# Optimization experiments

Hardware: AMD Instinct MI355X
Metric: run time of the kernel (lower is better)

The kernel has to match this reference:

```python
import jax, jax.numpy as jnp
import numpy as np

EPS = 1e-4
GRID_RES = 0.01
L = 2
ATOL = 0.01
RTOL = 1e-5


def compute_lub(f_v, edges):
    # f_v: [V,2] vertex filtration values; edges: [E,2] int vertex indices
    e_x = jnp.max(f_v[:, 0][edges], axis=1)  # [E]
    e_y = jnp.max(f_v[:, 1][edges], axis=1)  # [E]
    f_e = jnp.stack([e_x, e_y], axis=1) + EPS  # [E,2]
    return jnp.concatenate([f_v, f_e], axis=0)  # [V+E, 2] = [S,2]


def grad_matrices(filtration, bar, sample_pts):
    # filtration: [S,2], bar: [P,R], sample_pts: [P,2]
    # Vectorized version of the per-point Python loops in moveSimplices.forward.
    S = filtration.shape[0]
    P = sample_pts.shape[0]
    fx, fy = filtration[:, 0], filtration[:, 1]          # [S]
    px, py = sample_pts[:, 0], sample_pts[:, 1]          # [P]
    fsum = fx + fy                                        # [S]
    psum = px + py                                        # [P]
    shift = jnp.arange(-L, L + 1, dtype=filtration.dtype)  # [5]
    tol_x = ATOL + RTOL * jnp.abs(fx)                     # torch.isclose tolerance
    tol_y = ATOL + RTOL * jnp.abs(fy)
    below = fsum[None, :] < psum[:, None]                 # [P,S]
    above = fsum[None, :] > psum[:, None]

    Gs, Gcs = [], []
    for r in range(bar.shape[1]):  # small fixed rank loop (R=3)
        s = bar[:, r] + GRID_RES                          # [P]
        line_x = shift[None, :] * s[:, None] + px[:, None]  # [P,5]
        line_y = shift[None, :] * s[:, None] + py[:, None]
        last_x, last_y = line_x[:, -1], line_y[:, -1]      # [P] (shift=+L endpoint)
        # isclose over shifts, reduced with any() (duplicate scatter writes are idempotent)
        hit_x = (jnp.abs(line_x[:, None, :] - fx[None, :, None]) <= tol_x[None, :, None]).any(-1)  # [P,S]
        hit_y = (jnp.abs(line_y[:, None, :] - fy[None, :, None]) <= tol_y[None, :, None]).any(-1)
        lx = hit_x & (fy[None, :] <= last_y[:, None]) & below
        ux = hit_x & (fy[None, :] <= last_y[:, None]) & above
        ly = hit_y & (fx[None, :] <= last_x[:, None]) & below
        uy = hit_y & (fx[None, :] <= last_x[:, None]) & above
        vx = ux.astype(filtration.dtype) - lx.astype(filtration.dtype)  # +1 upper, -1 lower (exclusive)
        vy = uy.astype(filtration.dtype) - ly.astype(filtration.dtype)
        G = jnp.stack([vx, vy], axis=-1).reshape(P, 2 * S)  # interleave x,y columns
        cx = jnp.where(ux.any(1), -1.0, jnp.where(lx.any(1), 1.0, 0.0)).astype(filtration.dtype)
        cy = jnp.where(uy.any(1), -1.0, jnp.where(ly.any(1), 1.0, 0.0)).astype(filtration.dtype)
        Gc = jnp.stack([cx, cy], axis=-1)                  # [P,2]
        Gs.append(G)
        Gcs.append(Gc)
    return jnp.stack(Gs), jnp.stack(Gcs)  # [R,P,2S], [R,P,2]


def setup_inputs() -> dict:
    key = jax.random.key(0)
    k1, k2, k3, k4, k5 = jax.random.split(key, 5)
    V, E, P, R = 1200, 4800, 2500, 3
    f_v = jax.random.uniform(k1, (V, 2), dtype=jnp.float32)
    edges = jax.random.randint(k2, (E, 2), 0, V, dtype=jnp.int64)
    bars0 = jax.random.uniform(k3, (P, R), dtype=jnp.float32)
    bars1 = jax.random.uniform(k4, (P, R), dtype=jnp.float32)
    sample_pts = jax.random.uniform(k5, (P, 2), dtype=jnp.float32)
    return {"f_v": f_v, "edges": edges, "bars0": bars0, "bars1": bars1, "sample_pts": sample_pts}


def reference(f_v, edges, bars0, bars1, sample_pts):
    filtration = compute_lub(f_v, edges)
    G0, Gc0 = grad_matrices(filtration, bars0, sample_pts)
    G1, Gc1 = grad_matrices(filtration, bars1, sample_pts)
    # moveSimplices.forward returns the bars unchanged; the grad matrices are the
    # saved side outputs (ctx.grad_matrices_*) and the kernel-heavy computation.
    return (bars0, bars1, G0, G1, Gc0, Gc1)
```

## Files before the change

kernel.cpp:

```cpp
#include <hip/hip_runtime.h>

#define EPS_F      1e-4f
#define GRID_RES_F 0.01f
#define ATOL_F     0.01f
#define RTOL_F     1e-5f

static constexpr int V = 1200;
static constexpr int E = 4800;
static constexpr int S = V + E;
static constexpr int P = 2500;
static constexpr int R = 3;

static constexpr size_t G0_BASE  = 15000ull;
static constexpr size_t G_ELEMS  = (size_t)R * P * 2 * S;
static constexpr size_t GC0_BASE = G0_BASE + 2 * G_ELEMS;

__global__ void build_filt_kernel(const float* __restrict__ f_v,
                                  const int*   __restrict__ edges,
                                  float4*      __restrict__ filt) {
    int j = blockIdx.x * blockDim.x + threadIdx.x;
    if (j >= S) return;
    float fx, fy;
    if (j < V) {
        fx = f_v[2 * j];
        fy = f_v[2 * j + 1];
    } else {
        int e = j - V;
        int a = edges[2 * e];
        int b = edges[2 * e + 1];
        fx = __fadd_rn(fmaxf(f_v[2 * a],     f_v[2 * b]),     EPS_F);
        fy = __fadd_rn(fmaxf(f_v[2 * a + 1], f_v[2 * b + 1]), EPS_F);
    }
    float tolx = __fadd_rn(ATOL_F, __fmul_rn(RTOL_F, fabsf(fx)));
    float toly = __fadd_rn(ATOL_F, __fmul_rn(RTOL_F, fabsf(fy)));
    filt[j] = make_float4(fx, fy, tolx, toly);
}

__device__ __forceinline__ void cell(const float4 f, float psum,
                                     float last_x, float last_y,
                                     const float* lxs, const float* lys,
                                     float& vx, float& vy,
                                     int& aux, int& alx, int& auy, int& aly) {
    float fsum = __fadd_rn(f.x, f.y);
    bool below = fsum < psum;
    bool above = fsum > psum;
    bool hx = false, hy = false;
#pragma unroll
    for (int k = 0; k < 5; ++k) {
        hx = hx || (fabsf(__fsub_rn(lxs[k], f.x)) <= f.z);
        hy = hy || (fabsf(__fsub_rn(lys[k], f.y)) <= f.w);
    }
    bool condx = hx && (f.y <= last_y);
    bool condy = hy && (f.x <= last_x);
    bool ux = condx && above, lx = condx && below;
    bool uy = condy && above, ly = condy && below;
    vx = (ux ? 1.0f : 0.0f) - (lx ? 1.0f : 0.0f);
    vy = (uy ? 1.0f : 0.0f) - (ly ? 1.0f : 0.0f);
    aux |= (int)ux; alx |= (int)lx; auy |= (int)uy; aly |= (int)ly;
}

__global__ __launch_bounds__(256) void grad_kernel(
        const float4* __restrict__ filt,
        const float*  __restrict__ bars0,
        const float*  __restrict__ bars1,
        const float*  __restrict__ sample_pts,
        float*        __restrict__ d_out) {
    const int p = blockIdx.x;
    const int r = blockIdx.y;
    const int b = blockIdx.z;

    const float* bar = (b == 0) ? bars0 : bars1;
    const float px = sample_pts[2 * p];
    const float py = sample_pts[2 * p + 1];
    const float psum = __fadd_rn(px, py);
    const float s  = __fadd_rn(bar[p * R + r], GRID_RES_F);
    const float s2 = __fmul_rn(2.0f, s);

    float lxs[5], lys[5];
    lxs[0] = __fadd_rn(-s2, px); lxs[1] = __fadd_rn(-s, px); lxs[2] = px;
    lxs[3] = __fadd_rn( s, px);  lxs[4] = __fadd_rn(s2, px);
    lys[0] = __fadd_rn(-s2, py); lys[1] = __fadd_rn(-s, py); lys[2] = py;
    lys[3] = __fadd_rn( s, py);  lys[4] = __fadd_rn(s2, py);
    const float last_x = lxs[4];
    const float last_y = lys[4];

    float* Grow = d_out + G0_BASE + (size_t)b * G_ELEMS
                        + ((size_t)(r * P + p)) * (2 * S);

    __shared__ int sh_flags[4];
    if (threadIdx.x < 4) sh_flags[threadIdx.x] = 0;
    __syncthreads();

    int aux = 0, alx = 0, auy = 0, aly = 0;

    for (int j0 = threadIdx.x * 2; j0 < S; j0 += 512) {
        float4 f0 = filt[j0];
        float4 f1 = filt[j0 + 1];
        float4 o;
        cell(f0, psum, last_x, last_y, lxs, lys, o.x, o.y, aux, alx, auy, aly);
        cell(f1, psum, last_x, last_y, lxs, lys, o.z, o.w, aux, alx, auy, aly);
        *reinterpret_cast<float4*>(Grow + 2 * j0) = o;
    }

    if (aux) sh_flags[0] = 1;
    if (alx) sh_flags[1] = 1;
    if (auy) sh_flags[2] = 1;
    if (aly) sh_flags[3] = 1;
    __syncthreads();

    if (threadIdx.x == 0) {
        float cx = sh_flags[0] ? -1.0f : (sh_flags[1] ? 1.0f : 0.0f);
        float cy = sh_flags[2] ? -1.0f : (sh_flags[3] ? 1.0f : 0.0f);
        size_t gc = GC0_BASE + (size_t)b * ((size_t)R * P * 2)
                             + ((size_t)(r * P + p)) * 2;
        d_out[gc]     = cx;
        d_out[gc + 1] = cy;
    }
}

extern "C" void kernel_launch(void* const* d_in, const int* in_sizes, int n_in,
                              void* d_out, int out_size, void* d_ws, size_t ws_size,
                              hipStream_t stream) {
    const float* f_v        = (const float*)d_in[0];
    const int*   edges      = (const int*)d_in[1];
    const float* bars0      = (const float*)d_in[2];
    const float* bars1      = (const float*)d_in[3];
    const float* sample_pts = (const float*)d_in[4];
    float* out = (float*)d_out;

    float4* filt = (float4*)d_ws;

    hipMemcpyAsync(out,        bars0, (size_t)P * R * sizeof(float),
                   hipMemcpyDeviceToDevice, stream);
    hipMemcpyAsync(out + P * R, bars1, (size_t)P * R * sizeof(float),
                   hipMemcpyDeviceToDevice, stream);

    build_filt_kernel<<<(S + 255) / 256, 256, 0, stream>>>(f_v, edges, filt);

    dim3 grid(P, R, 2);
    grad_kernel<<<grid, 256, 0, stream>>>(filt, bars0, bars1, sample_pts, out);
}
```

Measured before the change: 731.2 us.

## Process all bar/rank rows per point in one block with nontemporal stores

Each block now handles all six (bar, rank) output rows for one sample point. Filtration loads and the above/below sign logic are reused across rows, and the hit test becomes a min-of-distances comparison. Output rows are written with nontemporal vector stores to avoid polluting caches, and the per-row flags are reduced through shared memory. The grid shrinks sixfold, which reduces the number of blocks available for latency hiding but raises per-thread work and stores in flight.

```diff
diff --git a/kernel.cpp b/kernel.cpp
--- a/kernel.cpp
+++ b/kernel.cpp
@@ -10,6 +10,9 @@
 static constexpr int S = V + E;
 static constexpr int P = 2500;
 static constexpr int R = 3;
+static constexpr int NROW = 2 * R;
+
+typedef float vfloat4 __attribute__((ext_vector_type(4)));
 
 static constexpr size_t G0_BASE  = 15000ull;
 static constexpr size_t G_ELEMS  = (size_t)R * P * 2 * S;
@@ -36,27 +39,28 @@
     filt[j] = make_float4(fx, fy, tolx, toly);
 }
 
-__device__ __forceinline__ void cell(const float4 f, float psum,
-                                     float last_x, float last_y,
-                                     const float* lxs, const float* lys,
-                                     float& vx, float& vy,
-                                     int& aux, int& alx, int& auy, int& aly) {
-    float fsum = __fadd_rn(f.x, f.y);
-    bool below = fsum < psum;
-    bool above = fsum > psum;
-    bool hx = false, hy = false;
-#pragma unroll
-    for (int k = 0; k < 5; ++k) {
-        hx = hx || (fabsf(__fsub_rn(lxs[k], f.x)) <= f.z);
-        hy = hy || (fabsf(__fsub_rn(lys[k], f.y)) <= f.w);
-    }
-    bool condx = hx && (f.y <= last_y);
-    bool condy = hy && (f.x <= last_x);
-    bool ux = condx && above, lx = condx && below;
-    bool uy = condy && above, ly = condy && below;
-    vx = (ux ? 1.0f : 0.0f) - (lx ? 1.0f : 0.0f);
-    vy = (uy ? 1.0f : 0.0f) - (ly ? 1.0f : 0.0f);
-    aux |= (int)ux; alx |= (int)lx; auy |= (int)uy; aly |= (int)ly;
+__device__ __forceinline__ float mindist(const float* l, float f) {
+    float a = fabsf(__fsub_rn(l[0], f));
+    float b = fabsf(__fsub_rn(l[1], f));
+    float c = fabsf(__fsub_rn(l[2], f));
+    float d = fabsf(__fsub_rn(l[3], f));
+    float e = fabsf(__fsub_rn(l[4], f));
+    return fminf(fminf(fminf(a, b), fminf(c, d)), e);
+}
+
+__device__ __forceinline__ void cellrow(const float4& f, float sg, bool ab, bool be,
+                                        const float* lxq, const float* lyq, int q,
+                                        float& vx, float& vy,
+                                        unsigned& fUx, unsigned& fLx,
+                                        unsigned& fUy, unsigned& fLy) {
+    bool cx = (mindist(lxq, f.x) <= f.z) && (f.y <= lyq[4]);
+    bool cy = (mindist(lyq, f.y) <= f.w) && (f.x <= lxq[4]);
+    vx = cx ? sg : 0.0f;
+    vy = cy ? sg : 0.0f;
+    if (cx && ab) fUx |= 1u << q;
+    if (cx && be) fLx |= 1u << q;
+    if (cy && ab) fUy |= 1u << q;
+    if (cy && be) fLy |= 1u << q;
 }
 
 __global__ __launch_bounds__(256) void grad_kernel(
@@ -66,51 +70,74 @@
         const float*  __restrict__ sample_pts,
         float*        __restrict__ d_out) {
     const int p = blockIdx.x;
-    const int r = blockIdx.y;
-    const int b = blockIdx.z;
 
-    const float* bar = (b == 0) ? bars0 : bars1;
     const float px = sample_pts[2 * p];
     const float py = sample_pts[2 * p + 1];
     const float psum = __fadd_rn(px, py);
-    const float s  = __fadd_rn(bar[p * R + r], GRID_RES_F);
-    const float s2 = __fmul_rn(2.0f, s);
 
-    float lxs[5], lys[5];
-    lxs[0] = __fadd_rn(-s2, px); lxs[1] = __fadd_rn(-s, px); lxs[2] = px;
-    lxs[3] = __fadd_rn( s, px);  lxs[4] = __fadd_rn(s2, px);
-    lys[0] = __fadd_rn(-s2, py); lys[1] = __fadd_rn(-s, py); lys[2] = py;
-    lys[3] = __fadd_rn( s, py);  lys[4] = __fadd_rn(s2, py);
-    const float last_x = lxs[4];
-    const float last_y = lys[4];
+    float lx[NROW][5], ly[NROW][5];
+#pragma unroll
+    for (int q = 0; q < NROW; ++q) {
+        const int b = q / R, r = q % R;
+        const float* bar = b ? bars1 : bars0;
+        float s  = __fadd_rn(bar[p * R + r], GRID_RES_F);
+        float s2 = __fmul_rn(2.0f, s);
+        lx[q][0] = __fadd_rn(-s2, px); lx[q][1] = __fadd_rn(-s, px);
+        lx[q][2] = px;
+        lx[q][3] = __fadd_rn( s, px);  lx[q][4] = __fadd_rn(s2, px);
+        ly[q][0] = __fadd_rn(-s2, py); ly[q][1] = __fadd_rn(-s, py);
+        ly[q][2] = py;
+        ly[q][3] = __fadd_rn( s, py);  ly[q][4] = __fadd_rn(s2, py);
+    }
 
-    float* Grow = d_out + G0_BASE + (size_t)b * G_ELEMS
+    float* grow[NROW];
+#pragma unroll
+    for (int q = 0; q < NROW; ++q) {
+        const int b = q / R, r = q % R;
+        grow[q] = d_out + G0_BASE + (size_t)b * G_ELEMS
                         + ((size_t)(r * P + p)) * (2 * S);
+    }
 
-    __shared__ int sh_flags[4];
-    if (threadIdx.x < 4) sh_flags[threadIdx.x] = 0;
-    __syncthreads();
-
-    int aux = 0, alx = 0, auy = 0, aly = 0;
+    unsigned fUx = 0, fLx = 0, fUy = 0, fLy = 0;
 
     for (int j0 = threadIdx.x * 2; j0 < S; j0 += 512) {
         float4 f0 = filt[j0];
         float4 f1 = filt[j0 + 1];
-        float4 o;
-        cell(f0, psum, last_x, last_y, lxs, lys, o.x, o.y, aux, alx, auy, aly);
-        cell(f1, psum, last_x, last_y, lxs, lys, o.z, o.w, aux, alx, auy, aly);
-        *reinterpret_cast<float4*>(Grow + 2 * j0) = o;
+        float fs0 = __fadd_rn(f0.x, f0.y);
+        float fs1 = __fadd_rn(f1.x, f1.y);
+        bool ab0 = fs0 > psum, be0 = fs0 < psum;
+        bool ab1 = fs1 > psum, be1 = fs1 < psum;
+        float sg0 = ab0 ? 1.0f : (be0 ? -1.0f : 0.0f);
+        float sg1 = ab1 ? 1.0f : (be1 ? -1.0f : 0.0f);
+#pragma unroll
+        for (int q = 0; q < NROW; ++q) {
+            float o0, o1, o2, o3;
+            cellrow(f0, sg0, ab0, be0, lx[q], ly[q], q, o0, o1,
+                    fUx, fLx, fUy, fLy);
+            cellrow(f1, sg1, ab1, be1, lx[q], ly[q], q, o2, o3,
+                    fUx, fLx, fUy, fLy);
+            vfloat4 o = {o0, o1, o2, o3};
+            __builtin_nontemporal_store(o,
+                reinterpret_cast<vfloat4*>(grow[q] + 2 * j0));
+        }
     }
 
-    if (aux) sh_flags[0] = 1;
-    if (alx) sh_flags[1] = 1;
-    if (auy) sh_flags[2] = 1;
-    if (aly) sh_flags[3] = 1;
+    __shared__ int shf[NROW * 4];
+    if (threadIdx.x < NROW * 4) shf[threadIdx.x] = 0;
+    __syncthreads();
+#pragma unroll
+    for (int q = 0; q < NROW; ++q) {
+        if ((fUx >> q) & 1) shf[q * 4 + 0] = 1;
+        if ((fLx >> q) & 1) shf[q * 4 + 1] = 1;
+        if ((fUy >> q) & 1) shf[q * 4 + 2] = 1;
+        if ((fLy >> q) & 1) shf[q * 4 + 3] = 1;
+    }
     __syncthreads();
 
-    if (threadIdx.x == 0) {
-        float cx = sh_flags[0] ? -1.0f : (sh_flags[1] ? 1.0f : 0.0f);
-        float cy = sh_flags[2] ? -1.0f : (sh_flags[3] ? 1.0f : 0.0f);
+    if (threadIdx.x < NROW) {
+        const int q = threadIdx.x, b = q / R, r = q % R;
+        float cx = shf[q * 4 + 0] ? -1.0f : (shf[q * 4 + 1] ? 1.0f : 0.0f);
+        float cy = shf[q * 4 + 2] ? -1.0f : (shf[q * 4 + 3] ? 1.0f : 0.0f);
         size_t gc = GC0_BASE + (size_t)b * ((size_t)R * P * 2)
                              + ((size_t)(r * P + p)) * 2;
         d_out[gc]     = cx;
@@ -130,13 +157,12 @@
 
     float4* filt = (float4*)d_ws;
 
-    hipMemcpyAsync(out,        bars0, (size_t)P * R * sizeof(float),
-                   hipMemcpyDeviceToDevice, stream);
-    hipMemcpyAsync(out + P * R, bars1, (size_t)P * R * sizeof(float),
-                   hipMemcpyDeviceToDevice, stream);
+    (void)hipMemcpyAsync(out,         bars0, (size_t)P * R * sizeof(float),
+                         hipMemcpyDeviceToDevice, stream);
+    (void)hipMemcpyAsync(out + P * R, bars1, (size_t)P * R * sizeof(float),
+                         hipMemcpyDeviceToDevice, stream);
 
     build_filt_kernel<<<(S + 255) / 256, 256, 0, stream>>>(f_v, edges, filt);
 
-    dim3 grid(P, R, 2);
-    grad_kernel<<<grid, 256, 0, stream>>>(filt, bars0, bars1, sample_pts, out);
+    grad_kernel<<<P, 256, 0, stream>>>(filt, bars0, bars1, sample_pts, out);
 }
```

Result: slower. 792.9 us (+8.4%).
